# Optimization experiments

Measured on AMD Instinct MI355X. Metric: run time of the kernel, lower is better.

## Reference

```python
import jax, jax.numpy as jnp
import numpy as np

IN_SIZE = 128
HID = 256
N_SRC1 = 500000
N_DST1 = 100000
E1 = 1600000
N_DST2 = 16384
E2 = 262144


def setup_inputs() -> dict:
    key = jax.random.key(0)
    ks = jax.random.split(key, 12)
    x = jax.random.normal(ks[0], (N_SRC1, IN_SIZE), dtype=jnp.float32)
    src1 = jax.random.randint(ks[1], (E1,), 0, N_SRC1, dtype=jnp.int32)
    dst1 = jax.random.randint(ks[2], (E1,), 0, N_DST1, dtype=jnp.int32)
    src2 = jax.random.randint(ks[3], (E2,), 0, N_DST1, dtype=jnp.int32)
    dst2 = jax.random.randint(ks[4], (E2,), 0, N_DST2, dtype=jnp.int32)
    s_in = 1.0 / np.sqrt(IN_SIZE)
    s_h = 1.0 / np.sqrt(HID)
    W_self1 = jax.random.normal(ks[5], (IN_SIZE, HID), dtype=jnp.float32) * s_in
    W_neigh1 = jax.random.normal(ks[6], (IN_SIZE, HID), dtype=jnp.float32) * s_in
    b1 = jnp.zeros((HID,), dtype=jnp.float32)
    W_self2 = jax.random.normal(ks[7], (HID, HID), dtype=jnp.float32) * s_h
    W_neigh2 = jax.random.normal(ks[8], (HID, HID), dtype=jnp.float32) * s_h
    b2 = jnp.zeros((HID,), dtype=jnp.float32)
    return {
        "x": x,
        "src1": src1, "dst1": dst1,
        "src2": src2, "dst2": dst2,
        "W_self1": W_self1, "W_neigh1": W_neigh1, "b1": b1,
        "W_self2": W_self2, "W_neigh2": W_neigh2, "b2": b2,
        "n_dst1": N_DST1, "n_dst2": N_DST2,
    }


def sage_conv_mean(h, src, dst, n_dst, W_self, W_neigh, b):
    # DGL block convention: dst nodes are the first n_dst src nodes.
    # mean aggregation over incoming neighbors (zero-degree -> 0 via deg clamp)
    msg_sum = jax.ops.segment_sum(h[src], dst, num_segments=n_dst)  # [n_dst, d]
    deg = jax.ops.segment_sum(jnp.ones(src.shape, h.dtype), dst, num_segments=n_dst)
    h_neigh = msg_sum / jnp.maximum(deg, 1.0)[:, None]
    return h[:n_dst] @ W_self + h_neigh @ W_neigh + b


def reference(x, src1, dst1, src2, dst2,
              W_self1, W_neigh1, b1, W_self2, W_neigh2, b2,
              n_dst1, n_dst2):
    h = sage_conv_mean(x, src1, dst1, n_dst1, W_self1, W_neigh1, b1)
    h = jax.nn.relu(h)  # relu between layers only
    h = sage_conv_mean(h, src2, dst2, n_dst2, W_self2, W_neigh2, b2)
    return h
```

## Files before the change

kernel.cpp:

```cpp
#include <hip/hip_runtime.h>

#define IN_SIZE 128
#define HID 256
#define N_SRC1 500000
#define N_DST1 100000
#define E1 1600000
#define N_DST2 16384
#define E2 262144

#define NBIN1 196
#define NBIN2 32
#define P1B1  800
#define P1B2  256

#define MB_HIST (P1B1 + P1B2)
#define MB_PACK 96
#define MB_CAST 2304
#define MB_TOTAL (MB_HIST + MB_PACK + MB_CAST)

#define OFF_XBF  0ull
#define OFF_H    128000000ull
#define OFF_MSG1 179200000ull
#define OFF_STG1 204800000ull
#define OFF_STG2 211200000ull
#define OFF_BP1  212248576ull
#define OFF_BP2  212875776ull
#define OFF_BT1  212908544ull
#define OFF_BT2  212909568ull
#define OFF_RP1  212912640ull
#define OFF_RP2  213312768ull
#define OFF_CSR1 213378432ull
#define OFF_CSR2 219778432ull
#define OFF_WP1  220827008ull
#define OFF_WP2  220958080ull

typedef __attribute__((ext_vector_type(8))) short short8;
typedef __attribute__((ext_vector_type(4))) float f32x4;

__device__ __forceinline__ unsigned short f2bf(float f) {
    unsigned u = __float_as_uint(f);
    return (unsigned short)((u + 0x7FFFu + ((u >> 16) & 1u)) >> 16);
}
__device__ __forceinline__ float bf2f(unsigned short b) {
    return __uint_as_float(((unsigned)b) << 16);
}

__global__ __launch_bounds__(256) void k_main1(
    const float* __restrict__ x, unsigned short* __restrict__ xbf,
    const int* __restrict__ dst1, int* __restrict__ hist1,
    const int* __restrict__ dst2, int* __restrict__ hist2,
    const float* __restrict__ Ws1, const float* __restrict__ Wn1,
    unsigned short* __restrict__ wp1,
    const float* __restrict__ Ws2, const float* __restrict__ Wn2,
    unsigned short* __restrict__ wp2)
{
    __shared__ int lcnt[NBIN1];
    const int bid = blockIdx.x;
    const int tid = threadIdx.x;

    if (bid < MB_HIST) {
        const bool l1 = bid < P1B1;
        const int blk = l1 ? bid : bid - P1B1;
        const int nbins = l1 ? NBIN1 : NBIN2;
        const int chunk = l1 ? (E1 / P1B1) : (E2 / P1B2);
        const int* dst = l1 ? dst1 : dst2;
        int* hist = l1 ? hist1 : hist2;
        const int e0 = blk * chunk;
        for (int i = tid; i < nbins; i += 256) lcnt[i] = 0;
        __syncthreads();
        for (int i = tid; i < chunk; i += 256)
            atomicAdd(&lcnt[dst[e0 + i] >> 9], 1);
        __syncthreads();
        for (int i = tid; i < nbins; i += 256)
            hist[blk * nbins + i] = lcnt[i];
    } else if (bid < MB_HIST + MB_PACK) {
        const int pb = bid - MB_HIST;
        const bool l1 = pb < 32;
        const int Keach = l1 ? 128 : 256;
        const float* Wa = l1 ? Ws1 : Ws2;
        const float* Wb = l1 ? Wn1 : Wn2;
        unsigned short* outp = l1 ? wp1 : wp2;
        const int t = (l1 ? pb : pb - 32) * 256 + tid;
        const int kb = t >> 10;
        const int c  = (t >> 2) & 255;
        const int g  = t & 3;
        const int kbase = kb * 32 + g * 8;
        const float* W = (kbase < Keach) ? (Wa + (size_t)kbase * HID + c)
                                         : (Wb + (size_t)(kbase - Keach) * HID + c);
        unsigned short* o = outp + ((size_t)kb * 256 + c) * 32 + g * 8;
        #pragma unroll
        for (int j = 0; j < 8; ++j) o[j] = f2bf(W[(size_t)j * HID]);
    } else {
        const int cb = bid - MB_HIST - MB_PACK;
        const int T = MB_CAST * 256;
        const float4* x4 = (const float4*)x;
        short8* o8 = (short8*)xbf;
        for (int i = cb * 256 + tid; i < N_SRC1 * IN_SIZE / 8; i += T) {
            const float4 u0 = x4[(size_t)i * 2];
            const float4 u1 = x4[(size_t)i * 2 + 1];
            short8 o;
            o[0] = (short)f2bf(u0.x); o[1] = (short)f2bf(u0.y);
            o[2] = (short)f2bf(u0.z); o[3] = (short)f2bf(u0.w);
            o[4] = (short)f2bf(u1.x); o[5] = (short)f2bf(u1.y);
            o[6] = (short)f2bf(u1.z); o[7] = (short)f2bf(u1.w);
            o8[i] = o;
        }
    }
}

__global__ __launch_bounds__(256) void k_scan_offs(
    const int* __restrict__ hist1, int* __restrict__ blkpref1, int* __restrict__ bintot1,
    const int* __restrict__ hist2, int* __restrict__ blkpref2, int* __restrict__ bintot2)
{
    __shared__ int s[256];
    const int tid = threadIdx.x;
    const bool l1 = blockIdx.x < NBIN1;
    const int b = l1 ? blockIdx.x : blockIdx.x - NBIN1;
    const int nblk = l1 ? P1B1 : P1B2;
    const int nbins = l1 ? NBIN1 : NBIN2;
    const int* hist = l1 ? hist1 : hist2;
    int* blkpref = l1 ? blkpref1 : blkpref2;
    int* bintot = l1 ? bintot1 : bintot2;

    int v[4];
    int lsum = 0;
    #pragma unroll
    for (int j = 0; j < 4; ++j) {
        const int idx = tid * 4 + j;
        v[j] = (idx < nblk) ? hist[idx * nbins + b] : 0;
        lsum += v[j];
    }
    s[tid] = lsum;
    __syncthreads();
    for (int off = 1; off < 256; off <<= 1) {
        int t = (tid >= off) ? s[tid - off] : 0;
        __syncthreads();
        s[tid] += t;
        __syncthreads();
    }
    int run = s[tid] - lsum;
    #pragma unroll
    for (int j = 0; j < 4; ++j) {
        const int idx = tid * 4 + j;
        if (idx < nblk) blkpref[idx * nbins + b] = run;
        run += v[j];
    }
    if (tid == 255) bintot[b] = s[255];
}

__global__ __launch_bounds__(256) void k_place(
    const int* __restrict__ src1, const int* __restrict__ dst1,
    const int* __restrict__ blkpref1, const int* __restrict__ bintot1,
    unsigned* __restrict__ stg1,
    const int* __restrict__ src2, const int* __restrict__ dst2,
    const int* __restrict__ blkpref2, const int* __restrict__ bintot2,
    unsigned* __restrict__ stg2)
{
    __shared__ int lcur[NBIN1];
    __shared__ int sp[256];
    const int tid = threadIdx.x;
    const bool l1 = blockIdx.x < P1B1;
    const int blk = l1 ? blockIdx.x : blockIdx.x - P1B1;
    const int nbins = l1 ? NBIN1 : NBIN2;
    const int chunk = l1 ? (E1 / P1B1) : (E2 / P1B2);
    const int* src = l1 ? src1 : src2;
    const int* dst = l1 ? dst1 : dst2;
    const int* blkpref = l1 ? blkpref1 : blkpref2;
    const int* bintot = l1 ? bintot1 : bintot2;
    unsigned* stg = l1 ? stg1 : stg2;
    const int e0 = blk * chunk;

    const int bv = (tid < nbins) ? bintot[tid] : 0;
    sp[tid] = bv;
    __syncthreads();
    for (int off = 1; off < 256; off <<= 1) {
        int t = (tid >= off) ? sp[tid - off] : 0;
        __syncthreads();
        sp[tid] += t;
        __syncthreads();
    }
    if (tid < nbins) lcur[tid] = (sp[tid] - bv) + blkpref[blk * nbins + tid];
    __syncthreads();

    for (int i = tid; i < chunk; i += 256) {
        const int e = e0 + i;
        const int d = dst[e];
        const unsigned pk = ((unsigned)(d & 511) << 19) | (unsigned)src[e];
        const int pos = atomicAdd(&lcur[d >> 9], 1);
        stg[pos] = pk;
    }
}

__global__ __launch_bounds__(512) void k_fill_p2b(
    const unsigned* __restrict__ stg1, const int* __restrict__ bintot1,
    int* __restrict__ rp1, int* __restrict__ csr1,
    const unsigned* __restrict__ stg2, const int* __restrict__ bintot2,
    int* __restrict__ rp2, int* __restrict__ csr2)
{
    __shared__ int lcnt[512];
    __shared__ int s[512];
    __shared__ int rbv[2];
    const int tid = threadIdx.x;
    const bool l1 = blockIdx.x < NBIN1;
    const int b = l1 ? blockIdx.x : blockIdx.x - NBIN1;
    const int base = b << 9;
    const int ndst = l1 ? N_DST1 : N_DST2;
    const int nbins = l1 ? NBIN1 : NBIN2;
    const int nr = min(512, ndst - base);
    const unsigned* stg = l1 ? stg1 : stg2;
    const int* bintot = l1 ? bintot1 : bintot2;
    int* rp = l1 ? rp1 : rp2;
    int* csr = l1 ? csr1 : csr2;

    const int bv = (tid < nbins) ? bintot[tid] : 0;
    s[tid] = bv;
    __syncthreads();
    for (int off = 1; off < 512; off <<= 1) {
        int t = (tid >= off) ? s[tid - off] : 0;
        __syncthreads();
        s[tid] += t;
        __syncthreads();
    }
    if (tid == b) { rbv[0] = s[tid] - bv; rbv[1] = s[tid]; }
    __syncthreads();
    const int s0 = rbv[0], s1 = rbv[1];

    lcnt[tid] = 0;
    __syncthreads();
    for (int i = s0 + tid; i < s1; i += 512)
        atomicAdd(&lcnt[stg[i] >> 19], 1);
    __syncthreads();

    const int v = lcnt[tid];
    s[tid] = v;
    __syncthreads();
    for (int off = 1; off < 512; off <<= 1) {
        int t = (tid >= off) ? s[tid - off] : 0;
        __syncthreads();
        s[tid] += t;
        __syncthreads();
    }
    const int excl = s0 + s[tid] - v;
    if (tid < nr) rp[base + tid] = excl;
    if (base + tid == ndst - 1) rp[ndst] = s1;
    __syncthreads();
    lcnt[tid] = excl;
    __syncthreads();

    for (int i = s0 + tid; i < s1; i += 512) {
        const unsigned pk = stg[i];
        const int pos = atomicAdd(&lcnt[pk >> 19], 1);
        csr[pos] = (int)(pk & 0x7FFFFu);
    }
}

__global__ __launch_bounds__(256) void k_pull1(
    const unsigned short* __restrict__ xbf, const int* __restrict__ rp,
    const int* __restrict__ csr, unsigned short* __restrict__ msg)
{
    const int d = blockIdx.x * 16 + (threadIdx.x >> 4);
    const int ql = threadIdx.x & 15;
    const int beg = rp[d], end = rp[d + 1];
    float a0 = 0.f, a1 = 0.f, a2 = 0.f, a3 = 0.f;
    float a4 = 0.f, a5 = 0.f, a6 = 0.f, a7 = 0.f;
    const unsigned short* xb = xbf + ql * 8;
    int j = beg;
    for (; j + 7 < end; j += 8) {
        const uint4 v0 = *(const uint4*)(xb + (size_t)csr[j + 0] * IN_SIZE);
        const uint4 v1 = *(const uint4*)(xb + (size_t)csr[j + 1] * IN_SIZE);
        const uint4 v2 = *(const uint4*)(xb + (size_t)csr[j + 2] * IN_SIZE);
        const uint4 v3 = *(const uint4*)(xb + (size_t)csr[j + 3] * IN_SIZE);
        const uint4 v4 = *(const uint4*)(xb + (size_t)csr[j + 4] * IN_SIZE);
        const uint4 v5 = *(const uint4*)(xb + (size_t)csr[j + 5] * IN_SIZE);
        const uint4 v6 = *(const uint4*)(xb + (size_t)csr[j + 6] * IN_SIZE);
        const uint4 v7 = *(const uint4*)(xb + (size_t)csr[j + 7] * IN_SIZE);
        a0 += ((bf2f(v0.x) + bf2f(v1.x)) + (bf2f(v2.x) + bf2f(v3.x)))
            + ((bf2f(v4.x) + bf2f(v5.x)) + (bf2f(v6.x) + bf2f(v7.x)));
        a1 += ((bf2f(v0.x >> 16) + bf2f(v1.x >> 16)) + (bf2f(v2.x >> 16) + bf2f(v3.x >> 16)))
            + ((bf2f(v4.x >> 16) + bf2f(v5.x >> 16)) + (bf2f(v6.x >> 16) + bf2f(v7.x >> 16)));
        a2 += ((bf2f(v0.y) + bf2f(v1.y)) + (bf2f(v2.y) + bf2f(v3.y)))
            + ((bf2f(v4.y) + bf2f(v5.y)) + (bf2f(v6.y) + bf2f(v7.y)));
        a3 += ((bf2f(v0.y >> 16) + bf2f(v1.y >> 16)) + (bf2f(v2.y >> 16) + bf2f(v3.y >> 16)))
            + ((bf2f(v4.y >> 16) + bf2f(v5.y >> 16)) + (bf2f(v6.y >> 16) + bf2f(v7.y >> 16)));
        a4 += ((bf2f(v0.z) + bf2f(v1.z)) + (bf2f(v2.z) + bf2f(v3.z)))
            + ((bf2f(v4.z) + bf2f(v5.z)) + (bf2f(v6.z) + bf2f(v7.z)));
        a5 += ((bf2f(v0.z >> 16) + bf2f(v1.z >> 16)) + (bf2f(v2.z >> 16) + bf2f(v3.z >> 16)))
            + ((bf2f(v4.z >> 16) + bf2f(v5.z >> 16)) + (bf2f(v6.z >> 16) + bf2f(v7.z >> 16)));
        a6 += ((bf2f(v0.w) + bf2f(v1.w)) + (bf2f(v2.w) + bf2f(v3.w)))
            + ((bf2f(v4.w) + bf2f(v5.w)) + (bf2f(v6.w) + bf2f(v7.w)));
        a7 += ((bf2f(v0.w >> 16) + bf2f(v1.w >> 16)) + (bf2f(v2.w >> 16) + bf2f(v3.w >> 16)))
            + ((bf2f(v4.w >> 16) + bf2f(v5.w >> 16)) + (bf2f(v6.w >> 16) + bf2f(v7.w >> 16)));
    }
    for (; j < end; ++j) {
        const uint4 v = *(const uint4*)(xb + (size_t)csr[j] * IN_SIZE);
        a0 += bf2f(v.x); a1 += bf2f(v.x >> 16);
        a2 += bf2f(v.y); a3 += bf2f(v.y >> 16);
        a4 += bf2f(v.z); a5 += bf2f(v.z >> 16);
        a6 += bf2f(v.w); a7 += bf2f(v.w >> 16);
    }
    const float inv = 1.0f / fmaxf((float)(end - beg), 1.0f);
    uint4 o;
    o.x = (unsigned)f2bf(a0 * inv) | ((unsigned)f2bf(a1 * inv) << 16);
    o.y = (unsigned)f2bf(a2 * inv) | ((unsigned)f2bf(a3 * inv) << 16);
    o.z = (unsigned)f2bf(a4 * inv) | ((unsigned)f2bf(a5 * inv) << 16);
    o.w = (unsigned)f2bf(a6 * inv) | ((unsigned)f2bf(a7 * inv) << 16);
    *(uint4*)(msg + (size_t)d * IN_SIZE + ql * 8) = o;
}

__global__ __launch_bounds__(256) void k_gemm1(
    const unsigned short* __restrict__ A1,
    const unsigned short* __restrict__ A2,
    const unsigned short* __restrict__ Wp,
    const float* __restrict__ bias,
    unsigned short* __restrict__ out)
{
    constexpr int NKS = 8;
    const int tid = threadIdx.x;
    const int wid = tid >> 6;
    const int lane = tid & 63;
    const int g = lane >> 4, r16 = lane & 15;
    const int i0 = blockIdx.x * 32;
    const int c0 = wid * 64;

    f32x4 acc[2][4];
    #pragma unroll
    for (int rb = 0; rb < 2; ++rb)
        #pragma unroll
        for (int cf = 0; cf < 4; ++cf)
            acc[rb][cf] = (f32x4){0.f, 0.f, 0.f, 0.f};

    #pragma unroll
    for (int ks = 0; ks < NKS; ++ks) {
        short8 a[2];
        #pragma unroll
        for (int rb = 0; rb < 2; ++rb) {
            const int row = i0 + rb * 16 + r16;
            const int kk = ks * 32 + g * 8;
            a[rb] = (ks < NKS / 2)
                ? *(const short8*)(A1 + (size_t)row * IN_SIZE + kk)
                : *(const short8*)(A2 + (size_t)row * IN_SIZE + (kk - IN_SIZE));
        }
        short8 b[4];
        #pragma unroll
        for (int cf = 0; cf < 4; ++cf) {
            const int col = c0 + cf * 16 + r16;
            b[cf] = *(const short8*)(Wp + ((size_t)ks * 256 + col) * 32 + g * 8);
        }
        #pragma unroll
        for (int rb = 0; rb < 2; ++rb)
            #pragma unroll
            for (int cf = 0; cf < 4; ++cf)
                acc[rb][cf] = __builtin_amdgcn_mfma_f32_16x16x32_bf16(
                    a[rb], b[cf], acc[rb][cf], 0, 0, 0);
    }

    #pragma unroll
    for (int cf = 0; cf < 4; ++cf) {
        const int col = c0 + cf * 16 + r16;
        const float bv = bias[col];
        #pragma unroll
        for (int rb = 0; rb < 2; ++rb)
            #pragma unroll
            for (int rr = 0; rr < 4; ++rr) {
                const int row = i0 + rb * 16 + g * 4 + rr;
                out[(size_t)row * HID + col] = f2bf(fmaxf(acc[rb][cf][rr] + bv, 0.0f));
            }
    }
}

__global__ __launch_bounds__(256) void k_sage2(
    const unsigned short* __restrict__ h,
    const int* __restrict__ rp, const int* __restrict__ csr,
    const unsigned short* __restrict__ Wp,
    const float* __restrict__ bias,
    float* __restrict__ out)
{
    __shared__ __align__(16) unsigned short At[32][264];
    const int tid = threadIdx.x;
    const int wid = tid >> 6;
    const int lane = tid & 63;
    const int i0 = blockIdx.x * 32;

    for (int r = 0; r < 8; ++r) {
        const int row = wid * 8 + r;
        const int d = i0 + row;
        const int beg = rp[d], end = rp[d + 1];
        float a0 = 0.f, a1 = 0.f, a2 = 0.f, a3 = 0.f;
        const unsigned short* hb = h + lane * 4;
        int j = beg;
        for (; j + 3 < end; j += 4) {
            const uint2 va = *(const uint2*)(hb + (size_t)csr[j + 0] * HID);
            const uint2 vb = *(const uint2*)(hb + (size_t)csr[j + 1] * HID);
            const uint2 vc = *(const uint2*)(hb + (size_t)csr[j + 2] * HID);
            const uint2 vd = *(const uint2*)(hb + (size_t)csr[j + 3] * HID);
            a0 += (bf2f(va.x) + bf2f(vb.x)) + (bf2f(vc.x) + bf2f(vd.x));
            a1 += (bf2f(va.x >> 16) + bf2f(vb.x >> 16)) + (bf2f(vc.x >> 16) + bf2f(vd.x >> 16));
            a2 += (bf2f(va.y) + bf2f(vb.y)) + (bf2f(vc.y) + bf2f(vd.y));
            a3 += (bf2f(va.y >> 16) + bf2f(vb.y >> 16)) + (bf2f(vc.y >> 16) + bf2f(vd.y >> 16));
        }
        for (; j < end; ++j) {
            const uint2 va = *(const uint2*)(hb + (size_t)csr[j] * HID);
            a0 += bf2f(va.x); a1 += bf2f(va.x >> 16);
            a2 += bf2f(va.y); a3 += bf2f(va.y >> 16);
        }
        const float inv = 1.0f / fmaxf((float)(end - beg), 1.0f);
        uint2 o;
        o.x = (unsigned)f2bf(a0 * inv) | ((unsigned)f2bf(a1 * inv) << 16);
        o.y = (unsigned)f2bf(a2 * inv) | ((unsigned)f2bf(a3 * inv) << 16);
        *(uint2*)&At[row][lane * 4] = o;
    }
    __syncthreads();

    const int g = lane >> 4, r16 = lane & 15;
    const int c0 = wid * 64;
    f32x4 acc[2][4];
    #pragma unroll
    for (int rb = 0; rb < 2; ++rb)
        #pragma unroll
        for (int cf = 0; cf < 4; ++cf)
            acc[rb][cf] = (f32x4){0.f, 0.f, 0.f, 0.f};

    #pragma unroll
    for (int ks = 0; ks < 16; ++ks) {
        short8 a[2];
        #pragma unroll
        for (int rb = 0; rb < 2; ++rb) {
            const int row16 = rb * 16 + r16;
            if (ks < 8)
                a[rb] = *(const short8*)(h + (size_t)(i0 + row16) * HID + ks * 32 + g * 8);
            else
                a[rb] = *(const short8*)&At[row16][(ks - 8) * 32 + g * 8];
        }
        short8 b[4];
        #pragma unroll
        for (int cf = 0; cf < 4; ++cf) {
            const int col = c0 + cf * 16 + r16;
            b[cf] = *(const short8*)(Wp + ((size_t)ks * 256 + col) * 32 + g * 8);
        }
        #pragma unroll
        for (int rb = 0; rb < 2; ++rb)
            #pragma unroll
            for (int cf = 0; cf < 4; ++cf)
                acc[rb][cf] = __builtin_amdgcn_mfma_f32_16x16x32_bf16(
                    a[rb], b[cf], acc[rb][cf], 0, 0, 0);
    }

    #pragma unroll
    for (int cf = 0; cf < 4; ++cf) {
        const int col = c0 + cf * 16 + r16;
        const float bv = bias[col];
        #pragma unroll
        for (int rb = 0; rb < 2; ++rb)
            #pragma unroll
            for (int rr = 0; rr < 4; ++rr) {
                const int row = i0 + rb * 16 + g * 4 + rr;
                out[(size_t)row * HID + col] = acc[rb][cf][rr] + bv;
            }
    }
}

extern "C" void kernel_launch(void* const* d_in, const int* in_sizes, int n_in,
                              void* d_out, int out_size, void* d_ws, size_t ws_size,
                              hipStream_t stream) {
    const float* x       = (const float*)d_in[0];
    const int*   src1    = (const int*)d_in[1];
    const int*   dst1    = (const int*)d_in[2];
    const int*   src2    = (const int*)d_in[3];
    const int*   dst2    = (const int*)d_in[4];
    const float* W_self1 = (const float*)d_in[5];
    const float* W_neigh1= (const float*)d_in[6];
    const float* b1      = (const float*)d_in[7];
    const float* W_self2 = (const float*)d_in[8];
    const float* W_neigh2= (const float*)d_in[9];
    const float* b2      = (const float*)d_in[10];
    float* out = (float*)d_out;

    char* ws = (char*)d_ws;
    unsigned short* xbf  = (unsigned short*)(ws + OFF_XBF);
    unsigned short* h    = (unsigned short*)(ws + OFF_H);
    unsigned short* msg1 = (unsigned short*)(ws + OFF_MSG1);
    unsigned* stg1 = (unsigned*)(ws + OFF_STG1);
    unsigned* stg2 = (unsigned*)(ws + OFF_STG2);
    int* bp1  = (int*)(ws + OFF_BP1);
    int* bp2  = (int*)(ws + OFF_BP2);
    int* bt1  = (int*)(ws + OFF_BT1);
    int* bt2  = (int*)(ws + OFF_BT2);
    int* rp1  = (int*)(ws + OFF_RP1);
    int* rp2  = (int*)(ws + OFF_RP2);
    int* csr1 = (int*)(ws + OFF_CSR1);
    int* csr2 = (int*)(ws + OFF_CSR2);
    unsigned short* wp1 = (unsigned short*)(ws + OFF_WP1);
    unsigned short* wp2 = (unsigned short*)(ws + OFF_WP2);

    k_main1<<<MB_TOTAL, 256, 0, stream>>>(x, xbf, dst1, bp1, dst2, bp2,
                                          W_self1, W_neigh1, wp1,
                                          W_self2, W_neigh2, wp2);
    k_scan_offs<<<NBIN1 + NBIN2, 256, 0, stream>>>(bp1, bp1, bt1, bp2, bp2, bt2);
    k_place<<<P1B1 + P1B2, 256, 0, stream>>>(src1, dst1, bp1, bt1, stg1,
                                             src2, dst2, bp2, bt2, stg2);
    k_fill_p2b<<<NBIN1 + NBIN2, 512, 0, stream>>>(stg1, bt1, rp1, csr1,
                                                  stg2, bt2, rp2, csr2);

    k_pull1<<<N_DST1 / 16, 256, 0, stream>>>(xbf, rp1, csr1, msg1);
    k_gemm1<<<N_DST1 / 32, 256, 0, stream>>>(xbf, msg1, wp1, b1, h);
    k_sage2<<<N_DST2 / 32, 256, 0, stream>>>(h, rp2, csr2, wp2, b2, out);
}
```

Baseline: 306.1 us.

## Spread x-to-bf16 cast across four CSR-build kernels to overlap latency-bound stages

The fp32-to-bf16 cast of x is split into four equal slices. Each slice is appended as extra blocks to one of the four CSR-construction kernels (histogram, scan, place, fill), so the bandwidth-heavy cast runs alongside the small, latency-bound scan and fill stages instead of all in the first kernel. This is meant to hide the cast's memory traffic behind stages that leave the GPU underutilised. The risk is that cast blocks compete with the critical-path blocks for compute units and bandwidth and delay them.

```diff
diff --git a/kernel.cpp b/kernel.cpp
--- a/kernel.cpp
+++ b/kernel.cpp
@@ -13,10 +13,12 @@
 #define P1B1  800
 #define P1B2  256
 
-#define MB_HIST (P1B1 + P1B2)
-#define MB_PACK 96
-#define MB_CAST 2304
-#define MB_TOTAL (MB_HIST + MB_PACK + MB_CAST)
+#define GRP_TOTAL 8000000
+#define SLICE     2000000
+#define CAST_A    2048
+#define CAST_B    2048
+#define CAST_C    2048
+#define CAST_D    1024
 
 #define OFF_XBF  0ull
 #define OFF_H    128000000ull
@@ -45,7 +47,25 @@
     return __uint_as_float(((unsigned)b) << 16);
 }
 
-__global__ __launch_bounds__(256) void k_main1(
+__device__ __forceinline__ void cast_slice(const float* __restrict__ x,
+                                           unsigned short* __restrict__ xbf,
+                                           int idx0, int stride, int end)
+{
+    const float4* x4 = (const float4*)x;
+    short8* o8 = (short8*)xbf;
+    for (int i = idx0; i < end; i += stride) {
+        const float4 u0 = x4[(size_t)i * 2];
+        const float4 u1 = x4[(size_t)i * 2 + 1];
+        short8 o;
+        o[0] = (short)f2bf(u0.x); o[1] = (short)f2bf(u0.y);
+        o[2] = (short)f2bf(u0.z); o[3] = (short)f2bf(u0.w);
+        o[4] = (short)f2bf(u1.x); o[5] = (short)f2bf(u1.y);
+        o[6] = (short)f2bf(u1.z); o[7] = (short)f2bf(u1.w);
+        o8[i] = o;
+    }
+}
+
+__global__ __launch_bounds__(256) void k_fillA(
     const float* __restrict__ x, unsigned short* __restrict__ xbf,
     const int* __restrict__ dst1, int* __restrict__ hist1,
     const int* __restrict__ dst2, int* __restrict__ hist2,
@@ -58,7 +78,7 @@
     const int bid = blockIdx.x;
     const int tid = threadIdx.x;
 
-    if (bid < MB_HIST) {
+    if (bid < P1B1 + P1B2) {
         const bool l1 = bid < P1B1;
         const int blk = l1 ? bid : bid - P1B1;
         const int nbins = l1 ? NBIN1 : NBIN2;
@@ -73,8 +93,8 @@
         __syncthreads();
         for (int i = tid; i < nbins; i += 256)
             hist[blk * nbins + i] = lcnt[i];
-    } else if (bid < MB_HIST + MB_PACK) {
-        const int pb = bid - MB_HIST;
+    } else if (bid < P1B1 + P1B2 + 96) {
+        const int pb = bid - (P1B1 + P1B2);
         const bool l1 = pb < 32;
         const int Keach = l1 ? 128 : 256;
         const float* Wa = l1 ? Ws1 : Ws2;
@@ -91,29 +111,23 @@
         #pragma unroll
         for (int j = 0; j < 8; ++j) o[j] = f2bf(W[(size_t)j * HID]);
     } else {
-        const int cb = bid - MB_HIST - MB_PACK;
-        const int T = MB_CAST * 256;
-        const float4* x4 = (const float4*)x;
-        short8* o8 = (short8*)xbf;
-        for (int i = cb * 256 + tid; i < N_SRC1 * IN_SIZE / 8; i += T) {
-            const float4 u0 = x4[(size_t)i * 2];
-            const float4 u1 = x4[(size_t)i * 2 + 1];
-            short8 o;
-            o[0] = (short)f2bf(u0.x); o[1] = (short)f2bf(u0.y);
-            o[2] = (short)f2bf(u0.z); o[3] = (short)f2bf(u0.w);
-            o[4] = (short)f2bf(u1.x); o[5] = (short)f2bf(u1.y);
-            o[6] = (short)f2bf(u1.z); o[7] = (short)f2bf(u1.w);
-            o8[i] = o;
-        }
-    }
-}
-
-__global__ __launch_bounds__(256) void k_scan_offs(
+        const int cb = bid - (P1B1 + P1B2 + 96);
+        cast_slice(x, xbf, 0 * SLICE + cb * 256 + tid, CAST_A * 256, 1 * SLICE);
+    }
+}
+
+__global__ __launch_bounds__(256) void k_fillB(
     const int* __restrict__ hist1, int* __restrict__ blkpref1, int* __restrict__ bintot1,
-    const int* __restrict__ hist2, int* __restrict__ blkpref2, int* __restrict__ bintot2)
+    const int* __restrict__ hist2, int* __restrict__ blkpref2, int* __restrict__ bintot2,
+    const float* __restrict__ x, unsigned short* __restrict__ xbf)
 {
     __shared__ int s[256];
     const int tid = threadIdx.x;
+    if (blockIdx.x >= NBIN1 + NBIN2) {
+        const int cb = blockIdx.x - (NBIN1 + NBIN2);
+        cast_slice(x, xbf, 1 * SLICE + cb * 256 + tid, CAST_B * 256, 2 * SLICE);
+        return;
+    }
     const bool l1 = blockIdx.x < NBIN1;
     const int b = l1 ? blockIdx.x : blockIdx.x - NBIN1;
     const int nblk = l1 ? P1B1 : P1B2;
@@ -148,17 +162,23 @@
     if (tid == 255) bintot[b] = s[255];
 }
 
-__global__ __launch_bounds__(256) void k_place(
+__global__ __launch_bounds__(256) void k_fillC(
     const int* __restrict__ src1, const int* __restrict__ dst1,
     const int* __restrict__ blkpref1, const int* __restrict__ bintot1,
     unsigned* __restrict__ stg1,
     const int* __restrict__ src2, const int* __restrict__ dst2,
     const int* __restrict__ blkpref2, const int* __restrict__ bintot2,
-    unsigned* __restrict__ stg2)
+    unsigned* __restrict__ stg2,
+    const float* __restrict__ x, unsigned short* __restrict__ xbf)
 {
     __shared__ int lcur[NBIN1];
     __shared__ int sp[256];
     const int tid = threadIdx.x;
+    if (blockIdx.x >= P1B1 + P1B2) {
+        const int cb = blockIdx.x - (P1B1 + P1B2);
+        cast_slice(x, xbf, 2 * SLICE + cb * 256 + tid, CAST_C * 256, 3 * SLICE);
+        return;
+    }
     const bool l1 = blockIdx.x < P1B1;
     const int blk = l1 ? blockIdx.x : blockIdx.x - P1B1;
     const int nbins = l1 ? NBIN1 : NBIN2;
@@ -191,16 +211,22 @@
     }
 }
 
-__global__ __launch_bounds__(512) void k_fill_p2b(
+__global__ __launch_bounds__(512) void k_fillD(
     const unsigned* __restrict__ stg1, const int* __restrict__ bintot1,
     int* __restrict__ rp1, int* __restrict__ csr1,
     const unsigned* __restrict__ stg2, const int* __restrict__ bintot2,
-    int* __restrict__ rp2, int* __restrict__ csr2)
+    int* __restrict__ rp2, int* __restrict__ csr2,
+    const float* __restrict__ x, unsigned short* __restrict__ xbf)
 {
     __shared__ int lcnt[512];
     __shared__ int s[512];
     __shared__ int rbv[2];
     const int tid = threadIdx.x;
+    if (blockIdx.x >= NBIN1 + NBIN2) {
+        const int cb = blockIdx.x - (NBIN1 + NBIN2);
+        cast_slice(x, xbf, 3 * SLICE + cb * 512 + tid, CAST_D * 512, 4 * SLICE);
+        return;
+    }
     const bool l1 = blockIdx.x < NBIN1;
     const int b = l1 ? blockIdx.x : blockIdx.x - NBIN1;
     const int base = b << 9;
@@ -492,14 +518,15 @@
     unsigned short* wp1 = (unsigned short*)(ws + OFF_WP1);
     unsigned short* wp2 = (unsigned short*)(ws + OFF_WP2);
 
-    k_main1<<<MB_TOTAL, 256, 0, stream>>>(x, xbf, dst1, bp1, dst2, bp2,
-                                          W_self1, W_neigh1, wp1,
-                                          W_self2, W_neigh2, wp2);
-    k_scan_offs<<<NBIN1 + NBIN2, 256, 0, stream>>>(bp1, bp1, bt1, bp2, bp2, bt2);
-    k_place<<<P1B1 + P1B2, 256, 0, stream>>>(src1, dst1, bp1, bt1, stg1,
-                                             src2, dst2, bp2, bt2, stg2);
-    k_fill_p2b<<<NBIN1 + NBIN2, 512, 0, stream>>>(stg1, bt1, rp1, csr1,
-                                                  stg2, bt2, rp2, csr2);
+    k_fillA<<<P1B1 + P1B2 + 96 + CAST_A, 256, 0, stream>>>(
+        x, xbf, dst1, bp1, dst2, bp2,
+        W_self1, W_neigh1, wp1, W_self2, W_neigh2, wp2);
+    k_fillB<<<NBIN1 + NBIN2 + CAST_B, 256, 0, stream>>>(
+        bp1, bp1, bt1, bp2, bp2, bt2, x, xbf);
+    k_fillC<<<P1B1 + P1B2 + CAST_C, 256, 0, stream>>>(
+        src1, dst1, bp1, bt1, stg1, src2, dst2, bp2, bt2, stg2, x, xbf);
+    k_fillD<<<NBIN1 + NBIN2 + CAST_D, 512, 0, stream>>>(
+        stg1, bt1, rp1, csr1, stg2, bt2, rp2, csr2, x, xbf);
 
     k_pull1<<<N_DST1 / 16, 256, 0, stream>>>(xbf, rp1, csr1, msg1);
     k_gemm1<<<N_DST1 / 32, 256, 0, stream>>>(xbf, msg1, wp1, b1, h);
```

After: 289.0 us (median of 2 runs). 5.6% less time.
